# Optimization experiments

Hardware: AMD Instinct MI355X
Metric: run time of the kernel (lower is better)

## Reference

```python
import jax, jax.numpy as jnp
import numpy as np

B, N, K, NUM_CLASSES = 8, 4096, 16, 40
M = B * N


def _safe_norm(v):
    s = jnp.sum(v * v, axis=-1)
    return jnp.where(s > 0, jnp.sqrt(jnp.where(s > 0, s, 1.0)), 0.0)


def _angle(v1, v2):
    cn = _safe_norm(jnp.cross(v1, v2))
    d = jnp.sum(v1 * v2, axis=-1)
    ok = (cn > 0) | (d != 0)
    return jnp.where(ok, jnp.arctan2(cn, jnp.where(ok, d, 1.0)), 0.0)


def _ppf(pos_i, pos_j, n_i, n_j):
    # PyG point_pair_features: pseudo = pos_j - pos_i (j = source, i = target)
    pseudo = pos_j - pos_i
    return jnp.stack([_safe_norm(pseudo), _angle(n_i, pseudo),
                      _angle(n_j, pseudo), _angle(n_i, n_j)], axis=-1)


def _knn_edges(pos):
    # knn_graph(k=K, loop=False), per-graph; returns (src, dst) with self-loops
    # appended (PPFConv add_self_loops=True default).
    p = pos.reshape(B, N, 3)
    sq = jnp.sum(p * p, axis=-1)                                   # [B,N]
    d2 = sq[:, :, None] + sq[:, None, :] - 2.0 * jnp.einsum('bnd,bmd->bnm', p, p)
    d2 = jnp.where(jnp.eye(N, dtype=bool)[None], jnp.inf, d2)      # no loops
    _, nbr = jax.lax.top_k(-d2, K)                                  # [B,N,K]
    offs = (jnp.arange(B) * N)[:, None, None]
    src = (nbr + offs).reshape(-1)                                  # neighbors j
    dst = jnp.repeat(jnp.arange(M), K)                              # targets i
    loops = jnp.arange(M)
    return jnp.concatenate([src, loops]), jnp.concatenate([dst, loops])


def _mlp(e, w1, b1, w2, b2):
    return jax.nn.relu(e @ w1 + b1) @ w2 + b2


def setup_inputs() -> dict:
    key = jax.random.key(0)
    ks = jax.random.split(key, 12)
    pos = jax.random.normal(ks[0], (M, 3), jnp.float32)
    nrm = jax.random.normal(ks[1], (M, 3), jnp.float32)
    nrm = nrm / jnp.linalg.norm(nrm, axis=-1, keepdims=True)
    batch = jnp.repeat(jnp.arange(B, dtype=jnp.int32), N)
    s = 0.1
    return {
        'pos': pos, 'normal': nrm, 'batch': batch,
        'w1a': jax.random.normal(ks[2], (4, 32)) * s,  'b1a': jnp.zeros(32),
        'w1b': jax.random.normal(ks[3], (32, 32)) * s, 'b1b': jnp.zeros(32),
        'w2a': jax.random.normal(ks[4], (36, 32)) * s, 'b2a': jnp.zeros(32),
        'w2b': jax.random.normal(ks[5], (32, 32)) * s, 'b2b': jnp.zeros(32),
        'wc':  jax.random.normal(ks[6], (32, NUM_CLASSES)) * s,
        'bc':  jnp.zeros(NUM_CLASSES),
    }


def reference(pos, normal, batch, w1a, b1a, w1b, b1b, w2a, b2a, w2b, b2b, wc, bc):
    src, dst = _knn_edges(pos)
    feats = _ppf(pos[dst], pos[src], normal[dst], normal[src])      # [E,4]
    # conv1: x=None -> message = mlp1(ppf), scatter-max per target node
    msg1 = _mlp(feats, w1a, b1a, w1b, b1b)
    x = jax.nn.relu(jax.ops.segment_max(msg1, dst, num_segments=M))  # [M,32]
    # conv2: message = mlp2([x_j, ppf])
    msg2 = _mlp(jnp.concatenate([x[src], feats], axis=-1), w2a, b2a, w2b, b2b)
    x = jax.nn.relu(jax.ops.segment_max(msg2, dst, num_segments=M))
    # global_max_pool over each graph (uniform batch: reshape)
    g = x.reshape(B, N, 32).max(axis=1)                              # [B,32]
    return g @ wc + bc                                               # [B,40]
```

## Files before the change

### kernel.cpp

```cpp
#include <hip/hip_runtime.h>
#include <hip/hip_bf16.h>
#include <math.h>

#define NB 8
#define NN 4096
#define KK 16
#define MM (NB*NN)
#define CH 32
#define SLOTS 17
#define NCLS 40
#define BIG 3.0e38f
#define CAP 96

#define OW1A 0
#define OB1A 128
#define OW1B 160
#define OB1B 1184
#define OW2A 1216
#define OB2A 2368
#define OW2B 2400
#define OB2B 3424
#define OWC  3456
#define OBC  4736
#define NWTS 4776

__device__ float4 g_pos4[MM];
__device__ float4 g_nrm4[MM];
__device__ int    g_nbr[MM*KK];
__device__ float  g_u[MM*CH];
__device__ float  g_x2[MM*CH];
__device__ float  g_wts[NWTS];
__device__ unsigned int g_gmax[NB*CH];
__device__ int    g_isf32;

__device__ __forceinline__ float bf(const __hip_bfloat16 x) { return __bfloat162float(x); }

__device__ __forceinline__ float ldf(const void* p, int i, bool f32) {
  return f32 ? ((const float*)p)[i] : bf(((const __hip_bfloat16*)p)[i]);
}

__device__ __forceinline__ float angf(float ax, float ay, float az,
                                      float bx, float by, float bz) {
  float cx = ay*bz - az*by;
  float cy = az*bx - ax*bz;
  float cz = ax*by - ay*bx;
  float s  = cx*cx + cy*cy + cz*cz;
  float cn = s > 0.f ? sqrtf(s) : 0.f;
  float d  = ax*bx + ay*by + az*bz;
  return (cn > 0.f || d != 0.f) ? atan2f(cn, d) : 0.f;
}

__device__ __forceinline__ void ppf4(const float4 pi, const float4 ni,
                                     const float4 pj, const float4 nj, float* f) {
  float px = pj.x - pi.x, py = pj.y - pi.y, pz = pj.z - pi.z;
  float s = px*px + py*py + pz*pz;
  f[0] = s > 0.f ? sqrtf(s) : 0.f;
  f[1] = angf(ni.x, ni.y, ni.z, px, py, pz);
  f[2] = angf(nj.x, nj.y, nj.z, px, py, pz);
  f[3] = angf(ni.x, ni.y, ni.z, nj.x, nj.y, nj.z);
}

__device__ __forceinline__ unsigned int fkey(float f) {
  unsigned int u = __float_as_uint(f);
  return (u & 0x80000000u) ? ~u : (u | 0x80000000u);
}
__device__ __forceinline__ float funkey(unsigned int k) {
  unsigned int u = (k & 0x80000000u) ? (k ^ 0x80000000u) : ~k;
  return __uint_as_float(u);
}

__global__ __launch_bounds__(256) void wprep_kernel(
    const void* nrm, const void* w1a, const void* b1a, const void* w1b,
    const void* b1b, const void* w2a, const void* b2a, const void* w2b,
    const void* b2b, const void* wc, const void* bc) {
  __shared__ int sflag;
  const int tid = threadIdx.x;
  if (tid < 64) {
    const float* nf = (const float*)nrm;
    const __hip_bfloat16* nh = (const __hip_bfloat16*)nrm;
    float x = nf[3*tid], y = nf[3*tid+1], z = nf[3*tid+2];
    float ss = x*x + y*y + z*z;
    bool okf = (ss > 0.98f && ss < 1.02f);
    float a = bf(nh[3*tid]), b2 = bf(nh[3*tid+1]), c2 = bf(nh[3*tid+2]);
    float sb = a*a + b2*b2 + c2*c2;
    bool okb = (sb > 0.95f && sb < 1.05f);
    unsigned long long mf = __ballot(okf), mb = __ballot(okb);
    if (tid == 0) {
      sflag = (__popcll(mf) >= __popcll(mb)) ? 1 : 0;
      g_isf32 = sflag;
    }
  }
  __syncthreads();
  const bool f32 = sflag != 0;
  for (int i = tid; i < NB*CH; i += 256) g_gmax[i] = 0u;
  for (int i = tid; i < 128;  i += 256) g_wts[OW1A + i] = ldf(w1a, i, f32);
  for (int i = tid; i < 32;   i += 256) g_wts[OB1A + i] = ldf(b1a, i, f32);
  for (int i = tid; i < 1024; i += 256) g_wts[OW1B + i] = ldf(w1b, i, f32);
  for (int i = tid; i < 32;   i += 256) g_wts[OB1B + i] = ldf(b1b, i, f32);
  for (int i = tid; i < 1152; i += 256) g_wts[OW2A + i] = ldf(w2a, i, f32);
  for (int i = tid; i < 32;   i += 256) g_wts[OB2A + i] = ldf(b2a, i, f32);
  for (int i = tid; i < 1024; i += 256) g_wts[OW2B + i] = ldf(w2b, i, f32);
  for (int i = tid; i < 32;   i += 256) g_wts[OB2B + i] = ldf(b2b, i, f32);
  for (int i = tid; i < 1280; i += 256) g_wts[OWC  + i] = ldf(wc,  i, f32);
  for (int i = tid; i < 40;   i += 256) g_wts[OBC  + i] = ldf(bc,  i, f32);
}

__global__ __launch_bounds__(256) void prep_kernel(const void* __restrict__ pos,
                                                   const void* __restrict__ nrm) {
  const bool f32 = g_isf32 != 0;
  int i = blockIdx.x*256 + threadIdx.x;
  float x = ldf(pos, 3*i, f32), y = ldf(pos, 3*i+1, f32), z = ldf(pos, 3*i+2, f32);
  float sq = x*x + y*y + z*z;
  g_pos4[i] = make_float4(x, y, z, sq);
  float a = ldf(nrm, 3*i, f32), b = ldf(nrm, 3*i+1, f32), c = ldf(nrm, 3*i+2, f32);
  g_nrm4[i] = make_float4(a, b, c, 0.f);
}

__global__ __launch_bounds__(512) void knn_kernel() {
  __shared__ float sx[NN], sy[NN], sz[NN];
  __shared__ unsigned short ilst[64][CAP];
  __shared__ double dlst[8][CAP];
  __shared__ int    cnt[64];
  const int tid  = threadIdx.x;
  const int w    = tid >> 6, lane = tid & 63;
  const int blk  = blockIdx.x;
  const int b    = blk >> 6;
  const int qbw  = ((blk & 63) << 6) | (w << 3);
  const float4* bp = g_pos4 + b*NN;

  #pragma unroll
  for (int k = 0; k < 8; ++k) {
    int idx = k*512 + tid;
    float4 o = bp[idx];
    sx[idx] = o.x; sy[idx] = o.y; sz[idx] = o.z;
  }
  __syncthreads();

  float q2x[8], q2y[8], q2z[8];
  #pragma unroll
  for (int qq = 0; qq < 8; ++qq) {
    int qi = qbw + qq;
    q2x[qq] = -2.f*sx[qi]; q2y[qq] = -2.f*sy[qi]; q2z[qq] = -2.f*sz[qi];
  }

  float mn[8];
  #pragma unroll
  for (int qq = 0; qq < 8; ++qq) mn[qq] = BIG;
  #pragma unroll 4
  for (int it = 0; it < 64; ++it) {
    int idx = it*64 + lane;
    float ox = sx[idx], oy = sy[idx], oz = sz[idx];
    float ow = __builtin_fmaf(oz, oz, __builtin_fmaf(oy, oy, ox*ox));
    #pragma unroll
    for (int qq = 0; qq < 8; ++qq) {
      float d = __builtin_fmaf(q2x[qq], ox,
                __builtin_fmaf(q2y[qq], oy,
                __builtin_fmaf(q2z[qq], oz, ow)));
      mn[qq] = fminf(mn[qq], d);
    }
  }

  float Tf[8];
  #pragma unroll
  for (int qq = 0; qq < 8; ++qq) {
    unsigned int key = fkey(mn[qq]);
    unsigned int lo = 0u, hi = 0xFFFFFFFFu;
    #pragma unroll 1
    for (int s = 0; s < 32; ++s) {
      unsigned int mid = lo + ((hi - lo) >> 1);
      int c = (int)__popcll(__ballot(key <= mid));
      if (c >= 17) hi = mid; else lo = mid + 1;
    }
    float T = funkey(hi);
    Tf[qq] = T + 4e-5f + 1e-5f*fabsf(T);
  }

  if (lane < 8) cnt[(w<<3) | lane] = 0;

  #pragma unroll 4
  for (int it = 0; it < 64; ++it) {
    int idx = it*64 + lane;
    float ox = sx[idx], oy = sy[idx], oz = sz[idx];
    float ow = __builtin_fmaf(oz, oz, __builtin_fmaf(oy, oy, ox*ox));
    #pragma unroll
    for (int qq = 0; qq < 8; ++qq) {
      float d = __builtin_fmaf(q2x[qq], ox,
                __builtin_fmaf(q2y[qq], oy,
                __builtin_fmaf(q2z[qq], oz, ow)));
      if (d <= Tf[qq] && idx != qbw + qq) {
        int p = atomicAdd(&cnt[(w<<3)|qq], 1);
        if (p < CAP) ilst[(w<<3)|qq][p] = (unsigned short)idx;
      }
    }
  }

  #pragma unroll 1
  for (int qq = 0; qq < 8; ++qq) {
    const int qi = qbw + qq;
    const int m = min(cnt[(w<<3)|qq], CAP);
    const double mx = (double)sx[qi], my_ = (double)sy[qi], mz = (double)sz[qi];
    const double sqme = (mx*mx + my_*my_) + mz*mz;
    for (int e = lane; e < m; e += 64) {
      int ci = ilst[(w<<3)|qq][e];
      double ox = (double)sx[ci], oy = (double)sy[ci], oz = (double)sz[ci];
      double sqo = (ox*ox + oy*oy) + oz*oz;
      double dt  = (mx*ox + my_*oy) + mz*oz;
      dlst[w][e] = (sqme + sqo) - 2.0*dt;
    }
    for (int e = lane; e < m; e += 64) {
      double myd = dlst[w][e];
      int myi = ilst[(w<<3)|qq][e];
      int rank = 0;
      for (int o = 0; o < m; ++o) {
        double od = dlst[w][o];
        int oi = ilst[(w<<3)|qq][o];
        rank += (od < myd) || (od == myd && oi < myi);
      }
      if (rank < KK) g_nbr[(b*NN + qi)*KK + rank] = b*NN + myi;
    }
  }
}

__global__ __launch_bounds__(256) void conv1_kernel() {
  __shared__ __align__(16) float fe[136][4];
  __shared__ __align__(16) float h1s[8*SLOTS*CH];
  __shared__ __align__(16) float xs[8][CH];
  const int tid = threadIdx.x;
  const int c = tid & 31;
  const int node0 = blockIdx.x << 3;
  float w1a_c[4], w1b_c[32], w2a_c[32];
  #pragma unroll
  for (int f = 0; f < 4; ++f)  w1a_c[f] = g_wts[OW1A + f*CH + c];
  #pragma unroll
  for (int k = 0; k < 32; ++k) w1b_c[k] = g_wts[OW1B + k*CH + c];
  #pragma unroll
  for (int k = 0; k < 32; ++k) w2a_c[k] = g_wts[OW2A + k*CH + c];
  const float b1a_c = g_wts[OB1A + c], b1b_c = g_wts[OB1B + c];

  if (tid < 136) {
    int ns = tid / 17, slot = tid - ns*17;
    int i = node0 + ns;
    int j = (slot < KK) ? g_nbr[i*KK + slot] : i;
    ppf4(g_pos4[i], g_nrm4[i], g_pos4[j], g_nrm4[j], fe[tid]);
  }
  __syncthreads();
  #pragma unroll
  for (int it = 0; it < 17; ++it) {
    int idx = it*256 + tid;
    int e = idx >> 5;
    float4 f4 = *(const float4*)fe[e];
    float h = b1a_c + f4.x*w1a_c[0] + f4.y*w1a_c[1] + f4.z*w1a_c[2] + f4.w*w1a_c[3];
    h1s[idx] = fmaxf(h, 0.f);
  }
  __syncthreads();
  const int ns = tid >> 5;
  const int i  = node0 + ns;
  float acc = -BIG;
  #pragma unroll
  for (int slot = 0; slot < SLOTS; ++slot) {
    const float* hr = &h1s[(ns*SLOTS + slot)*CH];
    float msg = b1b_c;
    #pragma unroll
    for (int k4 = 0; k4 < 8; ++k4) {
      float4 h4 = *(const float4*)(hr + 4*k4);
      msg += h4.x*w1b_c[4*k4] + h4.y*w1b_c[4*k4+1] + h4.z*w1b_c[4*k4+2] + h4.w*w1b_c[4*k4+3];
    }
    acc = fmaxf(acc, msg);
  }
  xs[ns][c] = fmaxf(acc, 0.f);
  __syncthreads();
  float uu = 0.f;
  #pragma unroll
  for (int k4 = 0; k4 < 8; ++k4) {
    float4 x4 = *(const float4*)&xs[ns][4*k4];
    uu += x4.x*w2a_c[4*k4] + x4.y*w2a_c[4*k4+1] + x4.z*w2a_c[4*k4+2] + x4.w*w2a_c[4*k4+3];
  }
  g_u[i*CH + c] = uu;
}

__global__ __launch_bounds__(256) void conv2_kernel() {
  __shared__ __align__(16) float fe[136][4];
  __shared__ int jn[136];
  __shared__ __align__(16) float h2s[8*SLOTS*CH];
  const int tid = threadIdx.x;
  const int c = tid & 31;
  const int node0 = blockIdx.x << 3;
  float w2aL_c[4], w2b_c[32];
  #pragma unroll
  for (int f = 0; f < 4; ++f)  w2aL_c[f] = g_wts[OW2A + (CH + f)*CH + c];
  #pragma unroll
  for (int k = 0; k < 32; ++k) w2b_c[k] = g_wts[OW2B + k*CH + c];
  const float b2a_c = g_wts[OB2A + c], b2b_c = g_wts[OB2B + c];

  if (tid < 136) {
    int ns = tid / 17, slot = tid - ns*17;
    int i = node0 + ns;
    int j = (slot < KK) ? g_nbr[i*KK + slot] : i;
    jn[tid] = j;
    ppf4(g_pos4[i], g_nrm4[i], g_pos4[j], g_nrm4[j], fe[tid]);
  }
  __syncthreads();
  #pragma unroll
  for (int it = 0; it < 17; ++it) {
    int idx = it*256 + tid;
    int e = idx >> 5;
    float4 f4 = *(const float4*)fe[e];
    float uv = g_u[jn[e]*CH + c];
    float h = b2a_c + uv + f4.x*w2aL_c[0] + f4.y*w2aL_c[1] + f4.z*w2aL_c[2] + f4.w*w2aL_c[3];
    h2s[idx] = fmaxf(h, 0.f);
  }
  __syncthreads();
  const int ns = tid >> 5;
  float acc = -BIG;
  #pragma unroll
  for (int slot = 0; slot < SLOTS; ++slot) {
    const float* hr = &h2s[(ns*SLOTS + slot)*CH];
    float msg = b2b_c;
    #pragma unroll
    for (int k4 = 0; k4 < 8; ++k4) {
      float4 h4 = *(const float4*)(hr + 4*k4);
      msg += h4.x*w2b_c[4*k4] + h4.y*w2b_c[4*k4+1] + h4.z*w2b_c[4*k4+2] + h4.w*w2b_c[4*k4+3];
    }
    acc = fmaxf(acc, msg);
  }
  g_x2[(node0 + ns)*CH + c] = fmaxf(acc, 0.f);
}

__global__ __launch_bounds__(256) void pmax_kernel() {
  __shared__ float red[8][CH];
  const int g = blockIdx.x >> 5;
  const int chunk = blockIdx.x & 31;
  const int c = threadIdx.x & 31, sub = threadIdx.x >> 5;
  const float* base = g_x2 + (size_t)(g*NN + chunk*128)*CH;
  float mx = 0.f;
  #pragma unroll
  for (int n = 0; n < 16; ++n)
    mx = fmaxf(mx, base[(n*8 + sub)*CH + c]);
  red[sub][c] = mx;
  __syncthreads();
  if (threadIdx.x < CH) {
    float m2 = red[0][c];
    #pragma unroll
    for (int r = 1; r < 8; ++r) m2 = fmaxf(m2, red[r][c]);
    atomicMax(&g_gmax[g*CH + c], __float_as_uint(m2));
  }
}

__global__ __launch_bounds__(64) void head_kernel(float* __restrict__ out) {
  const int g = blockIdx.x;
  const int co = threadIdx.x;
  if (co < NCLS) {
    float s = g_wts[OBC + co];
    #pragma unroll
    for (int f = 0; f < CH; ++f)
      s += __uint_as_float(g_gmax[g*CH + f]) * g_wts[OWC + f*NCLS + co];
    out[g*NCLS + co] = s;
  }
}

extern "C" void kernel_launch(void* const* d_in, const int* in_sizes, int n_in,
                              void* d_out, int out_size, void* d_ws, size_t ws_size,
                              hipStream_t stream) {
  const void* pos = d_in[0];
  const void* nrm = d_in[1];
  const void* w1a = d_in[3];
  const void* b1a = d_in[4];
  const void* w1b = d_in[5];
  const void* b1b = d_in[6];
  const void* w2a = d_in[7];
  const void* b2a = d_in[8];
  const void* w2b = d_in[9];
  const void* b2b = d_in[10];
  const void* wc  = d_in[11];
  const void* bc  = d_in[12];

  wprep_kernel<<<1,      256, 0, stream>>>(nrm, w1a, b1a, w1b, b1b, w2a, b2a, w2b, b2b, wc, bc);
  prep_kernel <<<MM/256, 256, 0, stream>>>(pos, nrm);
  knn_kernel  <<<MM/64,  512, 0, stream>>>();
  conv1_kernel<<<MM/8,   256, 0, stream>>>();
  conv2_kernel<<<MM/8,   256, 0, stream>>>();
  pmax_kernel <<<NB*32,  256, 0, stream>>>();
  head_kernel <<<NB,     64,  0, stream>>>((float*)d_out);
}
```

Baseline: 231.9 us.

## Precompute edge PPF features once, fuse global max pool into conv2, interleave KNN bisection

```diff
diff --git a/kernel.cpp b/kernel.cpp
--- a/kernel.cpp
+++ b/kernel.cpp
@@ -8,6 +8,7 @@
 #define MM (NB*NN)
 #define CH 32
 #define SLOTS 17
+#define NE (MM*SLOTS)
 #define NCLS 40
 #define BIG 3.0e38f
 #define CAP 96
@@ -27,8 +28,9 @@
 __device__ float4 g_pos4[MM];
 __device__ float4 g_nrm4[MM];
 __device__ int    g_nbr[MM*KK];
+__device__ float4 g_fe[NE];
+__device__ int    g_jn[NE];
 __device__ float  g_u[MM*CH];
-__device__ float  g_x2[MM*CH];
 __device__ float  g_wts[NWTS];
 __device__ unsigned int g_gmax[NB*CH];
 __device__ int    g_isf32;
@@ -48,16 +50,6 @@
   float cn = s > 0.f ? sqrtf(s) : 0.f;
   float d  = ax*bx + ay*by + az*bz;
   return (cn > 0.f || d != 0.f) ? atan2f(cn, d) : 0.f;
-}
-
-__device__ __forceinline__ void ppf4(const float4 pi, const float4 ni,
-                                     const float4 pj, const float4 nj, float* f) {
-  float px = pj.x - pi.x, py = pj.y - pi.y, pz = pj.z - pi.z;
-  float s = px*px + py*py + pz*pz;
-  f[0] = s > 0.f ? sqrtf(s) : 0.f;
-  f[1] = angf(ni.x, ni.y, ni.z, px, py, pz);
-  f[2] = angf(nj.x, nj.y, nj.z, px, py, pz);
-  f[3] = angf(ni.x, ni.y, ni.z, nj.x, nj.y, nj.z);
 }
 
 __device__ __forceinline__ unsigned int fkey(float f) {
@@ -160,18 +152,22 @@
     }
   }
 
+  unsigned int key[8], lo[8], hi[8];
+  #pragma unroll
+  for (int qq = 0; qq < 8; ++qq) { key[qq] = fkey(mn[qq]); lo[qq] = 0u; hi[qq] = 0xFFFFFFFFu; }
+  #pragma unroll 1
+  for (int s = 0; s < 32; ++s) {
+    #pragma unroll
+    for (int qq = 0; qq < 8; ++qq) {
+      unsigned int mid = lo[qq] + ((hi[qq] - lo[qq]) >> 1);
+      int c = (int)__popcll(__ballot(key[qq] <= mid));
+      if (c >= 17) hi[qq] = mid; else lo[qq] = mid + 1;
+    }
+  }
   float Tf[8];
   #pragma unroll
   for (int qq = 0; qq < 8; ++qq) {
-    unsigned int key = fkey(mn[qq]);
-    unsigned int lo = 0u, hi = 0xFFFFFFFFu;
-    #pragma unroll 1
-    for (int s = 0; s < 32; ++s) {
-      unsigned int mid = lo + ((hi - lo) >> 1);
-      int c = (int)__popcll(__ballot(key <= mid));
-      if (c >= 17) hi = mid; else lo = mid + 1;
-    }
-    float T = funkey(hi);
+    float T = funkey(hi[qq]);
     Tf[qq] = T + 4e-5f + 1e-5f*fabsf(T);
   }
 
@@ -221,6 +217,22 @@
   }
 }
 
+__global__ __launch_bounds__(256) void edges_kernel() {
+  int e = blockIdx.x*256 + threadIdx.x;
+  int i = e / SLOTS, slot = e - i*SLOTS;
+  int j = (slot < KK) ? g_nbr[i*KK + slot] : i;
+  g_jn[e] = j;
+  float4 pi = g_pos4[i], ni = g_nrm4[i];
+  float4 pj = g_pos4[j], nj = g_nrm4[j];
+  float px = pj.x - pi.x, py = pj.y - pi.y, pz = pj.z - pi.z;
+  float s = px*px + py*py + pz*pz;
+  float f0 = s > 0.f ? sqrtf(s) : 0.f;
+  float f1 = angf(ni.x, ni.y, ni.z, px, py, pz);
+  float f2 = angf(nj.x, nj.y, nj.z, px, py, pz);
+  float f3 = angf(ni.x, ni.y, ni.z, nj.x, nj.y, nj.z);
+  g_fe[e] = make_float4(f0, f1, f2, f3);
+}
+
 __global__ __launch_bounds__(256) void conv1_kernel() {
   __shared__ __align__(16) float fe[136][4];
   __shared__ __align__(16) float h1s[8*SLOTS*CH];
@@ -237,12 +249,7 @@
   for (int k = 0; k < 32; ++k) w2a_c[k] = g_wts[OW2A + k*CH + c];
   const float b1a_c = g_wts[OB1A + c], b1b_c = g_wts[OB1B + c];
 
-  if (tid < 136) {
-    int ns = tid / 17, slot = tid - ns*17;
-    int i = node0 + ns;
-    int j = (slot < KK) ? g_nbr[i*KK + slot] : i;
-    ppf4(g_pos4[i], g_nrm4[i], g_pos4[j], g_nrm4[j], fe[tid]);
-  }
+  if (tid < 136) *(float4*)fe[tid] = g_fe[node0*SLOTS + tid];
   __syncthreads();
   #pragma unroll
   for (int it = 0; it < 17; ++it) {
@@ -282,6 +289,7 @@
   __shared__ __align__(16) float fe[136][4];
   __shared__ int jn[136];
   __shared__ __align__(16) float h2s[8*SLOTS*CH];
+  __shared__ float xs[8][CH];
   const int tid = threadIdx.x;
   const int c = tid & 31;
   const int node0 = blockIdx.x << 3;
@@ -293,11 +301,8 @@
   const float b2a_c = g_wts[OB2A + c], b2b_c = g_wts[OB2B + c];
 
   if (tid < 136) {
-    int ns = tid / 17, slot = tid - ns*17;
-    int i = node0 + ns;
-    int j = (slot < KK) ? g_nbr[i*KK + slot] : i;
-    jn[tid] = j;
-    ppf4(g_pos4[i], g_nrm4[i], g_pos4[j], g_nrm4[j], fe[tid]);
+    *(float4*)fe[tid] = g_fe[node0*SLOTS + tid];
+    jn[tid] = g_jn[node0*SLOTS + tid];
   }
   __syncthreads();
   #pragma unroll
@@ -323,25 +328,13 @@
     }
     acc = fmaxf(acc, msg);
   }
-  g_x2[(node0 + ns)*CH + c] = fmaxf(acc, 0.f);
-}
-
-__global__ __launch_bounds__(256) void pmax_kernel() {
-  __shared__ float red[8][CH];
-  const int g = blockIdx.x >> 5;
-  const int chunk = blockIdx.x & 31;
-  const int c = threadIdx.x & 31, sub = threadIdx.x >> 5;
-  const float* base = g_x2 + (size_t)(g*NN + chunk*128)*CH;
-  float mx = 0.f;
-  #pragma unroll
-  for (int n = 0; n < 16; ++n)
-    mx = fmaxf(mx, base[(n*8 + sub)*CH + c]);
-  red[sub][c] = mx;
-  __syncthreads();
-  if (threadIdx.x < CH) {
-    float m2 = red[0][c];
-    #pragma unroll
-    for (int r = 1; r < 8; ++r) m2 = fmaxf(m2, red[r][c]);
+  xs[ns][c] = fmaxf(acc, 0.f);
+  __syncthreads();
+  if (tid < CH) {
+    float m2 = xs[0][c];
+    #pragma unroll
+    for (int r = 1; r < 8; ++r) m2 = fmaxf(m2, xs[r][c]);
+    int g = blockIdx.x >> 9;
     atomicMax(&g_gmax[g*CH + c], __float_as_uint(m2));
   }
 }
@@ -374,11 +367,11 @@
   const void* wc  = d_in[11];
   const void* bc  = d_in[12];
 
-  wprep_kernel<<<1,      256, 0, stream>>>(nrm, w1a, b1a, w1b, b1b, w2a, b2a, w2b, b2b, wc, bc);
-  prep_kernel <<<MM/256, 256, 0, stream>>>(pos, nrm);
-  knn_kernel  <<<MM/64,  512, 0, stream>>>();
-  conv1_kernel<<<MM/8,   256, 0, stream>>>();
-  conv2_kernel<<<MM/8,   256, 0, stream>>>();
-  pmax_kernel <<<NB*32,  256, 0, stream>>>();
-  head_kernel <<<NB,     64,  0, stream>>>((float*)d_out);
-}
+  wprep_kernel<<<1,       256, 0, stream>>>(nrm, w1a, b1a, w1b, b1b, w2a, b2a, w2b, b2b, wc, bc);
+  prep_kernel <<<MM/256,  256, 0, stream>>>(pos, nrm);
+  knn_kernel  <<<MM/64,   512, 0, stream>>>();
+  edges_kernel<<<NE/256,  256, 0, stream>>>();
+  conv1_kernel<<<MM/8,    256, 0, stream>>>();
+  conv2_kernel<<<MM/8,    256, 0, stream>>>();
+  head_kernel <<<NB,      64,  0, stream>>>((float*)d_out);
+}
```

New measurement: 250.6 us. +8.0%, slower.

## Fuse global max pool into conv2 and interleave kNN threshold bisection

Applied to the files above, without the earlier changes.

```diff
diff --git a/kernel.cpp b/kernel.cpp
--- a/kernel.cpp
+++ b/kernel.cpp
@@ -28,7 +28,6 @@
 __device__ float4 g_nrm4[MM];
 __device__ int    g_nbr[MM*KK];
 __device__ float  g_u[MM*CH];
-__device__ float  g_x2[MM*CH];
 __device__ float  g_wts[NWTS];
 __device__ unsigned int g_gmax[NB*CH];
 __device__ int    g_isf32;
@@ -160,18 +159,22 @@
     }
   }
 
+  unsigned int key[8], lo[8], hi[8];
+  #pragma unroll
+  for (int qq = 0; qq < 8; ++qq) { key[qq] = fkey(mn[qq]); lo[qq] = 0u; hi[qq] = 0xFFFFFFFFu; }
+  #pragma unroll 1
+  for (int s = 0; s < 32; ++s) {
+    #pragma unroll
+    for (int qq = 0; qq < 8; ++qq) {
+      unsigned int mid = lo[qq] + ((hi[qq] - lo[qq]) >> 1);
+      int c = (int)__popcll(__ballot(key[qq] <= mid));
+      if (c >= 17) hi[qq] = mid; else lo[qq] = mid + 1;
+    }
+  }
   float Tf[8];
   #pragma unroll
   for (int qq = 0; qq < 8; ++qq) {
-    unsigned int key = fkey(mn[qq]);
-    unsigned int lo = 0u, hi = 0xFFFFFFFFu;
-    #pragma unroll 1
-    for (int s = 0; s < 32; ++s) {
-      unsigned int mid = lo + ((hi - lo) >> 1);
-      int c = (int)__popcll(__ballot(key <= mid));
-      if (c >= 17) hi = mid; else lo = mid + 1;
-    }
-    float T = funkey(hi);
+    float T = funkey(hi[qq]);
     Tf[qq] = T + 4e-5f + 1e-5f*fabsf(T);
   }
 
@@ -282,6 +285,7 @@
   __shared__ __align__(16) float fe[136][4];
   __shared__ int jn[136];
   __shared__ __align__(16) float h2s[8*SLOTS*CH];
+  __shared__ float xs[8][CH];
   const int tid = threadIdx.x;
   const int c = tid & 31;
   const int node0 = blockIdx.x << 3;
@@ -323,25 +327,13 @@
     }
     acc = fmaxf(acc, msg);
   }
-  g_x2[(node0 + ns)*CH + c] = fmaxf(acc, 0.f);
-}
-
-__global__ __launch_bounds__(256) void pmax_kernel() {
-  __shared__ float red[8][CH];
-  const int g = blockIdx.x >> 5;
-  const int chunk = blockIdx.x & 31;
-  const int c = threadIdx.x & 31, sub = threadIdx.x >> 5;
-  const float* base = g_x2 + (size_t)(g*NN + chunk*128)*CH;
-  float mx = 0.f;
-  #pragma unroll
-  for (int n = 0; n < 16; ++n)
-    mx = fmaxf(mx, base[(n*8 + sub)*CH + c]);
-  red[sub][c] = mx;
-  __syncthreads();
-  if (threadIdx.x < CH) {
-    float m2 = red[0][c];
-    #pragma unroll
-    for (int r = 1; r < 8; ++r) m2 = fmaxf(m2, red[r][c]);
+  xs[ns][c] = fmaxf(acc, 0.f);
+  __syncthreads();
+  if (tid < CH) {
+    float m2 = xs[0][c];
+    #pragma unroll
+    for (int r = 1; r < 8; ++r) m2 = fmaxf(m2, xs[r][c]);
+    int g = blockIdx.x >> 9;
     atomicMax(&g_gmax[g*CH + c], __float_as_uint(m2));
   }
 }
@@ -379,6 +371,5 @@
   knn_kernel  <<<MM/64,  512, 0, stream>>>();
   conv1_kernel<<<MM/8,   256, 0, stream>>>();
   conv2_kernel<<<MM/8,   256, 0, stream>>>();
-  pmax_kernel <<<NB*32,  256, 0, stream>>>();
   head_kernel <<<NB,     64,  0, stream>>>((float*)d_out);
 }
```

Result: slower. 248.9 us (+7.3%).
